# Kernel tuning notes

Measured on AMD Instinct MI355X. Metric: run time of the kernel, lower is better.

The kernel has to match this reference:

```python
import jax, jax.numpy as jnp
import numpy as np
import math

DEGREE = 3
N_FEATURES = 16
BATCH = 262144
N_POLY = math.comb(N_FEATURES + DEGREE, DEGREE)  # 969


def _poly(x, degree):
    """Polynomial features up to `degree`, matching TaylorMap._poly ordering.

    Uses the Pascal-triangle column counts: for degree block d, feature i is
    multiplied against the first comb(d-1+i, d-1) columns of the previous block.
    Loops are over fixed degree/feature counts (unrolled at trace time).
    """
    n = x.shape[-1]
    b = x.shape[0]
    blocks = [jnp.ones((b, 1), x.dtype), x]
    for d in range(2, degree + 1):
        counts = [math.comb(d - 1 + j, d - 1) for j in range(n)]  # pascal row d-1
        last = blocks[-1]
        blocks.append(
            jnp.concatenate(
                [x[:, i : i + 1] * last[:, :m] for i, m in enumerate(counts)],
                axis=-1,
            )
        )
    return jnp.concatenate(blocks, axis=-1)  # [b, comb(n+degree, degree)]


def setup_inputs() -> dict:
    key = jax.random.key(0)
    kx, kw = jax.random.split(key)
    x = jax.random.normal(kx, (BATCH, N_FEATURES), dtype=jnp.float32)
    # W initialized small so the residual map stays well-conditioned
    W = jax.random.normal(kw, (N_POLY, N_FEATURES), dtype=jnp.float32) * 0.01
    return {"x": x, "W": W}


def reference(x, W):
    """TaylorMap forward: x + poly(x) @ W."""
    return x + _poly(x, DEGREE) @ W
```

## Files before the change

kernel.cpp:

```cpp
#include <hip/hip_runtime.h>

#define NSTEP 39
#define NCOL  (NSTEP * 8)

typedef _Float16 half8   __attribute__((ext_vector_type(8)));
typedef __fp16   f16x2   __attribute__((ext_vector_type(2)));
typedef __fp16   f16x4   __attribute__((ext_vector_type(4)));
typedef __fp16   f16x8   __attribute__((ext_vector_type(8)));
typedef float    float4v __attribute__((ext_vector_type(4)));

struct Cols { short mode[NCOL]; short a[NCOL]; short b[NCOL]; short o[NCOL]; };
static constexpr Cols mk_cols() {
  Cols c{};
  int k = 0;
  for (int o = 0; o < 16; o += 4) { c.mode[k] = 1; c.o[k] = (short)o; ++k; }
  c.mode[k] = 4; ++k;
  c.mode[k] = 0; ++k;
  for (int o = 0; o < 16; o += 4)
    for (int a = o; a < 16; ++a) { c.mode[k] = 2; c.a[k] = (short)a; c.o[k] = (short)o; ++k; }
  for (int o = 0; o < 16; o += 4) {
    const int amax = (o + 3 < 15) ? o + 3 : 15;
    for (int a = 0; a <= amax; ++a)
      for (int b = 0; b + 1 <= a; b += 2) {
        c.mode[k] = 3; c.a[k] = (short)a; c.b[k] = (short)b;     c.o[k] = (short)o; ++k;
        c.mode[k] = 3; c.a[k] = (short)a; c.b[k] = (short)(b+1); c.o[k] = (short)o; ++k;
      }
    for (int a = 0; a <= amax; a += 2) {
      c.mode[k] = 3; c.a[k] = (short)a; c.b[k] = (short)a; c.o[k] = (short)o; ++k;
    }
  }
  for (; k < NCOL; ++k) c.mode[k] = 0;
  return c;
}
static constexpr Cols COLS = mk_cols();

__global__ void build_wfrag(const float* __restrict__ W, _Float16* __restrict__ Wp) {
  const int e = blockIdx.x * 256 + threadIdx.x;
  if (e >= NSTEP * 64) return;
  const int step = e >> 6;
  const int q    = (e >> 4) & 3;
  const int n    = e & 15;
  half8 hv;
  #pragma unroll
  for (int j = 0; j < 8; ++j) {
    const int c = step * 8 + j;
    const int mode = COLS.mode[c], a = COLS.a[c], b = COLS.b[c], o = COLS.o[c];
    float v = 0.0f;
    if (mode == 3) {
      const int i = o + q;
      if (i >= a) v = W[(153 + i * (i + 1) * (i + 2) / 6 + a * (a + 1) / 2 + b) * 16 + n];
    } else if (mode == 2) {
      const int bb = o + q;
      if (bb <= a) v = W[(17 + a * (a + 1) / 2 + bb) * 16 + n];
    } else if (mode == 1) {
      const int i = o + q;
      v = W[(1 + i) * 16 + n];
      if (i == n) v += 1.0f;
    } else if (mode == 4) {
      if (q == 0) v = W[n];
    }
    hv[j] = (_Float16)v;
  }
  *(half8*)(Wp + e * 8) = hv;
}

template<int C>
__device__ __forceinline__ f16x2 colpair(const f16x2 (&x2)[8], const f16x2 (&w2)[4]) {
  constexpr int m0 = COLS.mode[C], m1 = COLS.mode[C + 1];
  if constexpr (m0 == 3 && COLS.a[C] == COLS.b[C]) {
    constexpr int a1 = COLS.a[C], a2 = COLS.a[C + 1];
    const f16x2 s = __builtin_shufflevector(x2[a1 / 2], x2[a2 / 2], a1 % 2, 2 + a2 % 2);
    return (s * s) * w2[COLS.o[C] >> 2];
  } else if constexpr (m0 == 3) {
    constexpr int a = COLS.a[C], b = COLS.b[C];
    const f16x2 xa = __builtin_shufflevector(x2[a / 2], x2[a / 2], a % 2, a % 2);
    return (xa * x2[b / 2]) * w2[COLS.o[C] >> 2];
  } else if constexpr (m0 == 2) {
    return x2[COLS.a[C] / 2] * w2[COLS.o[C] >> 2];
  } else if constexpr (m0 == 1 && m1 == 1) {
    return __builtin_shufflevector(w2[COLS.o[C] >> 2], w2[COLS.o[C + 1] >> 2], 0, 2);
  } else if constexpr (m0 == 4) {
    return (f16x2){(__fp16)1.0f, (__fp16)0.0f};
  } else {
    return (f16x2){(__fp16)0.0f, (__fp16)0.0f};
  }
}

template<int Q, int J>
__device__ __forceinline__ void setw2_one(const f16x2 (&x2)[8], f16x2 (&w2)[4]) {
  constexpr int idx = 4 * J + Q;
  w2[J] = __builtin_shufflevector(x2[idx / 2], x2[idx / 2], idx % 2, idx % 2);
}

template<int Q>
__device__ __forceinline__ void setw2(const f16x2 (&x2)[8], f16x2 (&w2)[4]) {
  setw2_one<Q, 0>(x2, w2); setw2_one<Q, 1>(x2, w2);
  setw2_one<Q, 2>(x2, w2); setw2_one<Q, 3>(x2, w2);
}

template<int S>
__device__ __forceinline__ void steps(const _Float16* __restrict__ wfq,
                                      const f16x2 (&x2)[8], const f16x2 (&w2)[4],
                                      float4v& acc) {
  if constexpr (S < NSTEP) {
    const half8 bf = *(const half8*)(wfq + S * 512);
    const f16x2 p01 = colpair<S * 8 + 0>(x2, w2);
    const f16x2 p23 = colpair<S * 8 + 2>(x2, w2);
    const f16x2 p45 = colpair<S * 8 + 4>(x2, w2);
    const f16x2 p67 = colpair<S * 8 + 6>(x2, w2);
    const f16x4 lo = __builtin_shufflevector(p01, p23, 0, 1, 2, 3);
    const f16x4 hi = __builtin_shufflevector(p45, p67, 0, 1, 2, 3);
    const f16x8 a8 = __builtin_shufflevector(lo, hi, 0, 1, 2, 3, 4, 5, 6, 7);
    const half8 af = __builtin_bit_cast(half8, a8);
    acc = __builtin_amdgcn_mfma_f32_16x16x32_f16(af, bf, acc, 0, 0, 0);
    steps<S + 1>(wfq, x2, w2, acc);
  }
}

__global__ __launch_bounds__(512, 8)
void taylor_fwd(const float* __restrict__ X, const _Float16* __restrict__ Wp,
                float* __restrict__ O) {
  __shared__ _Float16 wfrag[NSTEP * 512];
  const int tid  = threadIdx.x;
  const int lane = tid & 63;
  const int wv   = tid >> 6;
  const int m    = lane & 15;
  const int q    = lane >> 4;

  {
    float4v* dst = (float4v*)wfrag;
    const float4v* src = (const float4v*)Wp;
    #pragma unroll
    for (int i = 0; i < 5; ++i) {
      const int idx = tid + i * 512;
      if (idx < NSTEP * 64) dst[idx] = src[idx];
    }
  }
  __syncthreads();

  const int rb = blockIdx.x * 128 + wv * 16;
  f16x2 x2[8];
  {
    const float4v* xp = (const float4v*)(X + (size_t)(rb + m) * 16);
    #pragma unroll
    for (int c4 = 0; c4 < 4; ++c4) {
      const float4v v = xp[c4];
      x2[c4 * 2 + 0] = __builtin_amdgcn_cvt_pkrtz(v[0], v[1]);
      x2[c4 * 2 + 1] = __builtin_amdgcn_cvt_pkrtz(v[2], v[3]);
    }
  }

  f16x2 w2[4];
  if (q == 0)      setw2<0>(x2, w2);
  else if (q == 1) setw2<1>(x2, w2);
  else if (q == 2) setw2<2>(x2, w2);
  else             setw2<3>(x2, w2);

  float4v acc = (float4v){0.f, 0.f, 0.f, 0.f};

  const _Float16* wfq = wfrag + (q * 16 + m) * 8;
  steps<0>(wfq, x2, w2, acc);

  #pragma unroll
  for (int r = 0; r < 4; ++r) {
    const int row = rb + q * 4 + r;
    O[(size_t)row * 16 + m] = acc[r];
  }
}

extern "C" void kernel_launch(void* const* d_in, const int* in_sizes, int n_in,
                              void* d_out, int out_size, void* d_ws, size_t ws_size,
                              hipStream_t stream) {
  const float* X = (const float*)d_in[0];
  const float* W = (const float*)d_in[1];
  float*       O = (float*)d_out;
  _Float16*    Wp = (_Float16*)d_ws;
  const int batch = in_sizes[0] / 16;
  const int grid  = batch / 128;

  build_wfrag<<<(NSTEP * 64 + 255) / 256, 256, 0, stream>>>(W, Wp);
  taylor_fwd<<<grid, 512, 0, stream>>>(X, Wp, O);
}
```

Measured before the change: 86.64 us.

## Make kernel persistent with register-resident weight fragments and prefetched inputs

Replaces the one-tile-per-wave grid with a persistent grid of 512 blocks of 256 threads. Each wave loads all 39 weight B-fragments into registers once and loops over 16-row tiles, prefetching the next tile's inputs while computing the current one. This removes per-block shared-memory staging, the barrier and per-step LDS reads, and replaces the q-dependent branch for w2 with a byte-permute. The cost is heavy register pressure (39 half8 fragments) that limits occupancy and could cause spills, and reliance on the prefetch to hide global memory latency.

New measurement: 86.52 us. Within noise of the previous version (-0.1%).

```diff
diff --git a/kernel.cpp b/kernel.cpp
--- a/kernel.cpp
+++ b/kernel.cpp
@@ -86,24 +86,11 @@
   }
 }
 
-template<int Q, int J>
-__device__ __forceinline__ void setw2_one(const f16x2 (&x2)[8], f16x2 (&w2)[4]) {
-  constexpr int idx = 4 * J + Q;
-  w2[J] = __builtin_shufflevector(x2[idx / 2], x2[idx / 2], idx % 2, idx % 2);
-}
-
-template<int Q>
-__device__ __forceinline__ void setw2(const f16x2 (&x2)[8], f16x2 (&w2)[4]) {
-  setw2_one<Q, 0>(x2, w2); setw2_one<Q, 1>(x2, w2);
-  setw2_one<Q, 2>(x2, w2); setw2_one<Q, 3>(x2, w2);
-}
-
 template<int S>
-__device__ __forceinline__ void steps(const _Float16* __restrict__ wfq,
+__device__ __forceinline__ void steps(const half8 (&bfr)[NSTEP],
                                       const f16x2 (&x2)[8], const f16x2 (&w2)[4],
                                       float4v& acc) {
   if constexpr (S < NSTEP) {
-    const half8 bf = *(const half8*)(wfq + S * 512);
     const f16x2 p01 = colpair<S * 8 + 0>(x2, w2);
     const f16x2 p23 = colpair<S * 8 + 2>(x2, w2);
     const f16x2 p45 = colpair<S * 8 + 4>(x2, w2);
@@ -112,59 +99,81 @@
     const f16x4 hi = __builtin_shufflevector(p45, p67, 0, 1, 2, 3);
     const f16x8 a8 = __builtin_shufflevector(lo, hi, 0, 1, 2, 3, 4, 5, 6, 7);
     const half8 af = __builtin_bit_cast(half8, a8);
-    acc = __builtin_amdgcn_mfma_f32_16x16x32_f16(af, bf, acc, 0, 0, 0);
-    steps<S + 1>(wfq, x2, w2, acc);
+    acc = __builtin_amdgcn_mfma_f32_16x16x32_f16(af, bfr[S], acc, 0, 0, 0);
+    steps<S + 1>(bfr, x2, w2, acc);
   }
 }
 
-__global__ __launch_bounds__(512, 8)
+__global__ __launch_bounds__(256, 2)
 void taylor_fwd(const float* __restrict__ X, const _Float16* __restrict__ Wp,
-                float* __restrict__ O) {
-  __shared__ _Float16 wfrag[NSTEP * 512];
+                float* __restrict__ O, const int ntiles) {
   const int tid  = threadIdx.x;
   const int lane = tid & 63;
-  const int wv   = tid >> 6;
   const int m    = lane & 15;
   const int q    = lane >> 4;
+  const int wid  = blockIdx.x * 4 + (tid >> 6);
+  const int nw   = gridDim.x * 4;
 
+  half8 bfr[NSTEP];
   {
-    float4v* dst = (float4v*)wfrag;
-    const float4v* src = (const float4v*)Wp;
+    const _Float16* wpq = Wp + (size_t)(q * 16 + m) * 8;
     #pragma unroll
-    for (int i = 0; i < 5; ++i) {
-      const int idx = tid + i * 512;
-      if (idx < NSTEP * 64) dst[idx] = src[idx];
-    }
+    for (int S = 0; S < NSTEP; ++S)
+      bfr[S] = *(const half8*)(wpq + S * 512);
   }
-  __syncthreads();
 
-  const int rb = blockIdx.x * 128 + wv * 16;
-  f16x2 x2[8];
-  {
-    const float4v* xp = (const float4v*)(X + (size_t)(rb + m) * 16);
+  const unsigned psel = 0x01000100u + (unsigned)q * 0x02020202u;
+
+  int tile = wid;
+  float4v xv[4];
+  if (tile < ntiles) {
+    const float4v* xp = (const float4v*)(X + (size_t)(tile * 16 + m) * 16);
+    #pragma unroll
+    for (int c = 0; c < 4; ++c) xv[c] = xp[c];
+  }
+
+  while (tile < ntiles) {
+    const int next = tile + nw;
+
+    f16x2 x2[8];
     #pragma unroll
     for (int c4 = 0; c4 < 4; ++c4) {
-      const float4v v = xp[c4];
-      x2[c4 * 2 + 0] = __builtin_amdgcn_cvt_pkrtz(v[0], v[1]);
-      x2[c4 * 2 + 1] = __builtin_amdgcn_cvt_pkrtz(v[2], v[3]);
+      x2[c4 * 2 + 0] = __builtin_amdgcn_cvt_pkrtz(xv[c4][0], xv[c4][1]);
+      x2[c4 * 2 + 1] = __builtin_amdgcn_cvt_pkrtz(xv[c4][2], xv[c4][3]);
     }
-  }
 
-  f16x2 w2[4];
-  if (q == 0)      setw2<0>(x2, w2);
-  else if (q == 1) setw2<1>(x2, w2);
-  else if (q == 2) setw2<2>(x2, w2);
-  else             setw2<3>(x2, w2);
+    float4v xn[4];
+    if (next < ntiles) {
+      const float4v* xp = (const float4v*)(X + (size_t)(next * 16 + m) * 16);
+      #pragma unroll
+      for (int c = 0; c < 4; ++c) xn[c] = xp[c];
+    } else {
+      #pragma unroll
+      for (int c = 0; c < 4; ++c) xn[c] = (float4v){0.f, 0.f, 0.f, 0.f};
+    }
 
-  float4v acc = (float4v){0.f, 0.f, 0.f, 0.f};
+    f16x2 w2[4];
+    #pragma unroll
+    for (int j = 0; j < 4; ++j) {
+      const unsigned r = __builtin_amdgcn_perm(
+          __builtin_bit_cast(unsigned, x2[2 * j + 1]),
+          __builtin_bit_cast(unsigned, x2[2 * j]), psel);
+      w2[j] = __builtin_bit_cast(f16x2, r);
+    }
 
-  const _Float16* wfq = wfrag + (q * 16 + m) * 8;
-  steps<0>(wfq, x2, w2, acc);
+    float4v acc = (float4v){0.f, 0.f, 0.f, 0.f};
+    steps<0>(bfr, x2, w2, acc);
 
-  #pragma unroll
-  for (int r = 0; r < 4; ++r) {
-    const int row = rb + q * 4 + r;
-    O[(size_t)row * 16 + m] = acc[r];
+    const int rb = tile * 16;
+    #pragma unroll
+    for (int r = 0; r < 4; ++r) {
+      const int row = rb + q * 4 + r;
+      O[(size_t)row * 16 + m] = acc[r];
+    }
+
+    #pragma unroll
+    for (int c = 0; c < 4; ++c) xv[c] = xn[c];
+    tile = next;
   }
 }
 
@@ -175,9 +184,10 @@
   const float* W = (const float*)d_in[1];
   float*       O = (float*)d_out;
   _Float16*    Wp = (_Float16*)d_ws;
-  const int batch = in_sizes[0] / 16;
-  const int grid  = batch / 128;
+  const int batch  = in_sizes[0] / 16;
+  const int ntiles = batch / 16;
+  const int grid   = 512;
 
   build_wfrag<<<(NSTEP * 64 + 255) / 256, 256, 0, stream>>>(W, Wp);
-  taylor_fwd<<<grid, 512, 0, stream>>>(X, Wp, O);
+  taylor_fwd<<<grid, 256, 0, stream>>>(X, Wp, O, ntiles);
 }
```
